# Kernel optimization log

Measured on AMD Instinct MI355X. Metric: run time of the kernel, lower is better.

Reference implementation:

```python
import jax, jax.numpy as jnp
import numpy as np

B, N, C = 4, 2048, 1024
H = 16
D = C // H  # head_dim = 64
SCALE = 1.0 / np.sqrt(D).astype(np.float32)


def setup_inputs() -> dict:
    key = jax.random.key(0)
    ks = jax.random.split(key, 6)
    s = 0.02
    return {
        "x": jax.random.normal(ks[0], (B, N, C), dtype=jnp.float32),
        "Wq": jax.random.normal(ks[1], (C, C), dtype=jnp.float32) * s,
        "Wk": jax.random.normal(ks[2], (C, C), dtype=jnp.float32) * s,
        "Wv": jax.random.normal(ks[3], (C, C), dtype=jnp.float32) * s,
        "Wo": jax.random.normal(ks[4], (C, C), dtype=jnp.float32) * s,
        "bo": jax.random.normal(ks[5], (C,), dtype=jnp.float32) * s,
    }


def reference(x, Wq, Wk, Wv, Wo, bo):
    # q/k/v projections (no bias, qkv_bias=False), split heads -> [B,H,N,D]
    def heads(t):
        return t.reshape(B, N, H, D).transpose(0, 2, 1, 3)
    q = heads(x @ Wq)
    k = heads(x @ Wk)
    v = heads(x @ Wv)
    attn = jnp.einsum("bhnd,bhmd->bhnm", q, k) * SCALE  # [B,H,N,N]
    attn = jax.nn.softmax(attn, axis=-1)
    out = jnp.einsum("bhnm,bhmd->bhnd", attn, v)  # [B,H,N,D]
    out = out.transpose(0, 2, 1, 3).reshape(B, N, C)
    return out @ Wo + bo
```

## Files before the change

### kernel.cpp

```cpp
#include <hip/hip_runtime.h>
#include <hip/hip_bf16.h>


typedef __bf16 bf16x8 __attribute__((ext_vector_type(8)));
typedef __bf16 bf16x4 __attribute__((ext_vector_type(4)));
typedef float  f32x4  __attribute__((ext_vector_type(4)));
typedef unsigned int u32x4 __attribute__((ext_vector_type(4)));

#define LSCALE 0.18033688f

__device__ __forceinline__ f32x4 mfma16(bf16x8 a, bf16x8 b, f32x4 c) {
    return __builtin_amdgcn_mfma_f32_16x16x32_bf16(a, b, c, 0, 0, 0);
}

__device__ __forceinline__ unsigned short f2bf(float f) {
    unsigned u = __builtin_bit_cast(unsigned, f);
    u += 0x7fffu + ((u >> 16) & 1u);
    return (unsigned short)(u >> 16);
}

__device__ __forceinline__ unsigned cvt_pk_bf16(float lo, float hi) {
    unsigned r;
    asm("v_cvt_pk_bf16_f32 %0, %1, %2" : "=v"(r) : "v"(lo), "v"(hi));
    return r;
}

__device__ __forceinline__ bf16x4 trread(unsigned addr) {
    bf16x4 d;
    asm volatile("ds_read_b64_tr_b16 %0, %1" : "=v"(d) : "v"(addr));
    return d;
}

__device__ __forceinline__ void gload16(const ushort* g, ushort* l) {
    __builtin_amdgcn_global_load_lds(
        (const __attribute__((address_space(1))) void*)g,
        (__attribute__((address_space(3))) void*)l, 16, 0, 0);
}

__global__ void cast_bf16_kernel(const float4* __restrict__ in,
                                 ushort4* __restrict__ out, int n4) {
    int i = blockIdx.x * blockDim.x + threadIdx.x;
    if (i < n4) {
        float4 f = in[i];
        ushort4 r;
        r.x = f2bf(f.x); r.y = f2bf(f.y); r.z = f2bf(f.z); r.w = f2bf(f.w);
        out[i] = r;
    }
}

__global__ void transpose_cast_kernel(const float* __restrict__ Wq,
                                      const float* __restrict__ Wk,
                                      const float* __restrict__ Wv,
                                      const float* __restrict__ Wo,
                                      ushort* __restrict__ out) {
    __shared__ float tile[32][33];
    const int z = blockIdx.z;
    const float* W = (z == 0) ? Wq : (z == 1) ? Wk : (z == 2) ? Wv : Wo;
    ushort* o = out + (size_t)z * 1024 * 1024;
    const int k0 = blockIdx.x * 32, n0 = blockIdx.y * 32;
    const int tx = threadIdx.x, ty = threadIdx.y;
#pragma unroll
    for (int i = 0; i < 4; i++)
        tile[ty + 8 * i][tx] = W[(size_t)(k0 + ty + 8 * i) * 1024 + n0 + tx];
    __syncthreads();
#pragma unroll
    for (int i = 0; i < 4; i++)
        o[(size_t)(n0 + ty + 8 * i) * 1024 + k0 + tx] = f2bf(tile[tx][ty + 8 * i]);
}

template <int MODE>
__global__ __launch_bounds__(256) void gemm128(const ushort* __restrict__ A,
                                               const ushort* __restrict__ Bt,
                                               ushort* __restrict__ outB,
                                               float* __restrict__ outF,
                                               const float* __restrict__ bias) {
    __shared__ ushort As[128 * 32];
    __shared__ ushort Bs[128 * 32];
    const int tid = threadIdx.x;
    const int lane = tid & 63;
    const int wid = tid >> 6;
    const int wm = wid >> 1, wn = wid & 1;
    const int m0 = blockIdx.x * 128;
    const int n0 = blockIdx.y * 128;
    if (MODE == 0) Bt += (size_t)blockIdx.z * (1024 * 1024);

    f32x4 acc[4][4] = {};

    for (int k0 = 0; k0 < 1024; k0 += 32) {
#pragma unroll
        for (int it = 0; it < 2; ++it) {
            int e = (it * 256 + tid) * 8;
            int r = e >> 5, c = e & 31;
            gload16(&A[(size_t)(m0 + r) * 1024 + k0 + c], &As[e]);
            gload16(&Bt[(size_t)(n0 + r) * 1024 + k0 + c], &Bs[e]);
        }
        __syncthreads();

        bf16x8 a[4], b[4];
#pragma unroll
        for (int i = 0; i < 4; i++) {
            a[i] = *(const bf16x8*)&As[(wm * 64 + i * 16 + (lane & 15)) * 32 + (lane >> 4) * 8];
            b[i] = *(const bf16x8*)&Bs[(wn * 64 + i * 16 + (lane & 15)) * 32 + (lane >> 4) * 8];
        }
#pragma unroll
        for (int i = 0; i < 4; i++)
#pragma unroll
            for (int j = 0; j < 4; j++)
                acc[i][j] = mfma16(a[i], b[j], acc[i][j]);
        __syncthreads();
    }

    const float scl = (MODE == 0 && blockIdx.z == 0) ? LSCALE : 1.0f;
#pragma unroll
    for (int i = 0; i < 4; i++) {
        int row_b = m0 + wm * 64 + i * 16 + ((lane >> 4) * 4);
#pragma unroll
        for (int j = 0; j < 4; j++) {
            int col = n0 + wn * 64 + j * 16 + (lane & 15);
#pragma unroll
            for (int r = 0; r < 4; r++) {
                int row = row_b + r;
                float v = acc[i][j][r] * scl;
                if (MODE == 0) {
                    ushort* o = outB + (size_t)blockIdx.z * (8192ull * 1024);
                    int b = row >> 11, n = row & 2047, h = col >> 6, d = col & 63;
                    o[((((size_t)(b * 16 + h)) * 2048 + n) << 6) + d] = f2bf(v);
                } else {
                    outF[(size_t)row * 1024 + col] = v + bias[col];
                }
            }
        }
    }
}

__global__ __launch_bounds__(256) void attn_kernel(const ushort* __restrict__ Q,
                                                   const ushort* __restrict__ K,
                                                   const ushort* __restrict__ V,
                                                   ushort* __restrict__ O) {
    __shared__ ushort Ks[64 * 64];
    __shared__ ushort Vs[64 * 64];
    __shared__ ushort Ps[4][2][1024];
    const int tid = threadIdx.x;
    const int lane = tid & 63;
    const int wid = tid >> 6;
    const int g = lane >> 4;
    const int q16 = lane & 15;
    const int bid = blockIdx.x;
    const int swz = (bid & 7) * 128 + (bid >> 3);
    const int bh = swz >> 4;
    const int qt = swz & 15;
    const size_t base = (size_t)bh * (2048 * 64);

    const int qr0 = qt * 128 + wid * 32 + q16;
    bf16x8 qf[2][2];
#pragma unroll
    for (int u = 0; u < 2; ++u)
#pragma unroll
        for (int ks = 0; ks < 2; ++ks)
            qf[u][ks] = *(const bf16x8*)&Q[base + (size_t)(qr0 + u * 16) * 64 + ks * 32 + g * 8];

    bf16x8 onesb;
#pragma unroll
    for (int i = 0; i < 8; i++) onesb[i] = (__bf16)1.0f;

    f32x4 o[2][4] = {};
    f32x4 lacc[2] = {};
    float m_run[2] = {-1e30f, -1e30f};

    char* KsB = (char*)Ks;
    const unsigned vb = (unsigned)(size_t)&Vs[0];

    for (int kt = 0; kt < 2048; kt += 64) {
#pragma unroll
        for (int it = 0; it < 2; ++it) {
            int ci = it * 256 + tid;
            int key = ci >> 3, d0 = (ci & 7) * 8;
            uint4 kv = *(const uint4*)&K[base + (size_t)(kt + key) * 64 + d0];
            int byt = (key * 128 + d0 * 2) ^ ((key & 7) << 4);
            *(uint4*)(KsB + byt) = kv;
        }
#pragma unroll
        for (int it = 0; it < 2; ++it) {
            int c = it * 256 + tid;
            int key = (c & 127) >> 1;
            int d0 = (c >> 7) * 16 + (c & 1) * 8;
            gload16(&V[base + (size_t)(kt + key) * 64 + d0], &Vs[c * 8]);
        }
        __syncthreads();

        f32x4 s[2][4] = {};
#pragma unroll
        for (int kb = 0; kb < 4; ++kb) {
#pragma unroll
            for (int ks = 0; ks < 2; ++ks) {
                int key = kb * 16 + q16;
                int d0 = ks * 32 + g * 8;
                int byt = (key * 128 + d0 * 2) ^ ((key & 7) << 4);
                bf16x8 kf = *(const bf16x8*)(KsB + byt);
                s[0][kb] = mfma16(kf, qf[0][ks], s[0][kb]);
                s[1][kb] = mfma16(kf, qf[1][ks], s[1][kb]);
            }
        }

        bf16x8 pa[2][2];
#pragma unroll
        for (int u = 0; u < 2; ++u) {
            float t[4][4];
#pragma unroll
            for (int kb = 0; kb < 4; ++kb)
#pragma unroll
                for (int r = 0; r < 4; ++r) t[kb][r] = s[u][kb][r];

            float mx = fmaxf(fmaxf(fmaxf(t[0][0], t[0][1]), fmaxf(t[0][2], t[0][3])),
                             fmaxf(fmaxf(t[1][0], t[1][1]), fmaxf(t[1][2], t[1][3])));
            mx = fmaxf(mx, fmaxf(fmaxf(fmaxf(t[2][0], t[2][1]), fmaxf(t[2][2], t[2][3])),
                                 fmaxf(fmaxf(t[3][0], t[3][1]), fmaxf(t[3][2], t[3][3]))));
            mx = fmaxf(mx, __shfl_xor(mx, 16));
            mx = fmaxf(mx, __shfl_xor(mx, 32));
            float mn = fmaxf(m_run[u], mx);
            float fr = __builtin_amdgcn_exp2f(m_run[u] - mn);
            m_run[u] = mn;

            unsigned w[4][2];
#pragma unroll
            for (int kb = 0; kb < 4; ++kb) {
                float p0 = __builtin_amdgcn_exp2f(t[kb][0] - mn);
                float p1 = __builtin_amdgcn_exp2f(t[kb][1] - mn);
                float p2 = __builtin_amdgcn_exp2f(t[kb][2] - mn);
                float p3 = __builtin_amdgcn_exp2f(t[kb][3] - mn);
                w[kb][0] = cvt_pk_bf16(p0, p1);
                w[kb][1] = cvt_pk_bf16(p2, p3);
            }

            char* PsB = (char*)Ps[wid][u];
            {
                u32x4 c0 = {w[0][0], w[0][1], w[2][0], w[2][1]};
                u32x4 c1 = {w[1][0], w[1][1], w[3][0], w[3][1]};
                *(u32x4*)(PsB + ((lane * 32 + 0)  ^ ((lane & 7) << 4))) = c0;
                *(u32x4*)(PsB + ((lane * 32 + 16) ^ ((lane & 7) << 4))) = c1;
            }
            asm volatile("" ::: "memory");
            __builtin_amdgcn_sched_barrier(0);
            int s1 = q16 + 32 * (g & 1);
            int ch = (g >> 1) * 16;
            u32x4 r1 = *(const u32x4*)(PsB + ((s1 * 32 + ch) ^ ((s1 & 7) << 4)));
            u32x4 r2 = *(const u32x4*)(PsB + (((s1 + 16) * 32 + ch) ^ (((s1 + 16) & 7) << 4)));
            asm volatile("" ::: "memory");
            {
                u32x4 p0 = {r1.x, r1.y, r2.x, r2.y};
                u32x4 p1 = {r1.z, r1.w, r2.z, r2.w};
                pa[u][0] = __builtin_bit_cast(bf16x8, p0);
                pa[u][1] = __builtin_bit_cast(bf16x8, p1);
            }

            float fro[4];
#pragma unroll
            for (int r = 0; r < 4; ++r) fro[r] = __shfl(fr, g * 4 + r);
#pragma unroll
            for (int cb = 0; cb < 4; ++cb)
#pragma unroll
                for (int r = 0; r < 4; ++r) o[u][cb][r] *= fro[r];
#pragma unroll
            for (int r = 0; r < 4; ++r) lacc[u][r] *= fro[r];

            lacc[u] = mfma16(pa[u][0], onesb, lacc[u]);
            lacc[u] = mfma16(pa[u][1], onesb, lacc[u]);
        }

        bf16x4 vlo[4][2], vhi[4][2];
#pragma unroll
        for (int cb = 0; cb < 4; ++cb)
#pragma unroll
            for (int ks = 0; ks < 2; ++ks) {
                unsigned a = vb + cb * 2048 + (ks * 32 + g * 8) * 32 + q16 * 8;
                vlo[cb][ks] = trread(a);
                vhi[cb][ks] = trread(a + 128);
            }
        asm volatile("s_waitcnt lgkmcnt(0)" ::: "memory");
        __builtin_amdgcn_sched_barrier(0);
#pragma unroll
        for (int cb = 0; cb < 4; ++cb)
#pragma unroll
            for (int ks = 0; ks < 2; ++ks) {
                bf16x8 vf = __builtin_shufflevector(vlo[cb][ks], vhi[cb][ks],
                                                    0, 1, 2, 3, 4, 5, 6, 7);
                o[0][cb] = mfma16(pa[0][ks], vf, o[0][cb]);
                o[1][cb] = mfma16(pa[1][ks], vf, o[1][cb]);
            }
        __syncthreads();
    }

    const int b = bh >> 4, h = bh & 15;
#pragma unroll
    for (int u = 0; u < 2; ++u) {
#pragma unroll
        for (int r = 0; r < 4; ++r) {
            float inv = 1.0f / lacc[u][r];
            int row = qt * 128 + wid * 32 + u * 16 + g * 4 + r;
#pragma unroll
            for (int cb = 0; cb < 4; ++cb) {
                int col = h * 64 + cb * 16 + q16;
                O[((size_t)(b * 2048 + row)) * 1024 + col] = f2bf(o[u][cb][r] * inv);
            }
        }
    }
}

extern "C" void kernel_launch(void* const* d_in, const int* in_sizes, int n_in,
                              void* d_out, int out_size, void* d_ws, size_t ws_size,
                              hipStream_t stream) {
    const float* x  = (const float*)d_in[0];
    const float* Wq = (const float*)d_in[1];
    const float* Wk = (const float*)d_in[2];
    const float* Wv = (const float*)d_in[3];
    const float* Wo = (const float*)d_in[4];
    const float* bo = (const float*)d_in[5];
    float* out = (float*)d_out;

    if (ws_size < (size_t)72 * 1024 * 1024) return;
    ushort* ws  = (ushort*)d_ws;
    ushort* xb  = ws;
    ushort* wt  = xb + (size_t)8 * 1024 * 1024;
    ushort* qkv = wt + (size_t)4 * 1024 * 1024;
    ushort* ao  = xb;

    cast_bf16_kernel<<<8192, 256, 0, stream>>>((const float4*)x, (ushort4*)xb,
                                               2 * 1024 * 1024);
    transpose_cast_kernel<<<dim3(32, 32, 4), dim3(32, 8), 0, stream>>>(Wq, Wk, Wv, Wo, wt);
    gemm128<0><<<dim3(64, 8, 3), 256, 0, stream>>>(xb, wt, qkv, nullptr, nullptr);
    attn_kernel<<<1024, 256, 0, stream>>>(
        qkv, qkv + (size_t)8 * 1024 * 1024, qkv + (size_t)16 * 1024 * 1024, ao);
    gemm128<1><<<dim3(64, 8, 1), 256, 0, stream>>>(ao, wt + (size_t)3 * 1024 * 1024,
                                                   nullptr, out, bo);
}
```

Measured before the change: 242.0 us.

## Double-buffer K/V tiles in attention kernel to overlap loads with compute

Doubles the shared-memory K and V buffers and prefetches the next key tile during the current tile's computation. V goes in through async global-to-LDS loads, while K is held in registers and written to LDS after the PV MFMAs. This drops one barrier per iteration and is meant to hide global-load latency behind the MFMA work. The cost is more LDS (which may lower occupancy) and more registers for the prefetched K values. A possible hazard is the shared-memory wait count when the async V loads mix with the LDS reads in the same iteration.

Result: faster. 237.0 us (-2.1%).

```diff
diff --git a/kernel.cpp b/kernel.cpp
--- a/kernel.cpp
+++ b/kernel.cpp
@@ -137,8 +137,8 @@
                                                    const ushort* __restrict__ K,
                                                    const ushort* __restrict__ V,
                                                    ushort* __restrict__ O) {
-    __shared__ ushort Ks[64 * 64];
-    __shared__ ushort Vs[64 * 64];
+    __shared__ ushort Ks[2][64 * 64];
+    __shared__ ushort Vs[2][64 * 64];
     __shared__ ushort Ps[4][2][1024];
     const int tid = threadIdx.x;
     const int lane = tid & 63;
@@ -167,26 +167,43 @@
     f32x4 lacc[2] = {};
     float m_run[2] = {-1e30f, -1e30f};
 
-    char* KsB = (char*)Ks;
-    const unsigned vb = (unsigned)(size_t)&Vs[0];
-
+    const int kci0 = tid, kci1 = 256 + tid;
+    const int kkey0 = kci0 >> 3, kd0 = (kci0 & 7) * 8;
+    const int kkey1 = kci1 >> 3, kd1 = (kci1 & 7) * 8;
+    const int kbyt0 = (kkey0 * 128 + kd0 * 2) ^ ((kkey0 & 7) << 4);
+    const int kbyt1 = (kkey1 * 128 + kd1 * 2) ^ ((kkey1 & 7) << 4);
+    const int vkey0 = (kci0 & 127) >> 1, vd0 = (kci0 >> 7) * 16 + (kci0 & 1) * 8;
+    const int vkey1 = (kci1 & 127) >> 1, vd1 = (kci1 >> 7) * 16 + (kci1 & 1) * 8;
+
+    char* const KsB0 = (char*)&Ks[0][0];
+    ushort* const Vs0 = &Vs[0][0];
+    const unsigned vb0 = (unsigned)(size_t)&Vs[0][0];
+
+    {
+        uint4 k0 = *(const uint4*)&K[base + (size_t)kkey0 * 64 + kd0];
+        uint4 k1 = *(const uint4*)&K[base + (size_t)kkey1 * 64 + kd1];
+        gload16(&V[base + (size_t)vkey0 * 64 + vd0], &Vs0[kci0 * 8]);
+        gload16(&V[base + (size_t)vkey1 * 64 + vd1], &Vs0[kci1 * 8]);
+        *(uint4*)(KsB0 + kbyt0) = k0;
+        *(uint4*)(KsB0 + kbyt1) = k1;
+    }
+    __syncthreads();
+
+    int cur = 0;
     for (int kt = 0; kt < 2048; kt += 64) {
-#pragma unroll
-        for (int it = 0; it < 2; ++it) {
-            int ci = it * 256 + tid;
-            int key = ci >> 3, d0 = (ci & 7) * 8;
-            uint4 kv = *(const uint4*)&K[base + (size_t)(kt + key) * 64 + d0];
-            int byt = (key * 128 + d0 * 2) ^ ((key & 7) << 4);
-            *(uint4*)(KsB + byt) = kv;
-        }
-#pragma unroll
-        for (int it = 0; it < 2; ++it) {
-            int c = it * 256 + tid;
-            int key = (c & 127) >> 1;
-            int d0 = (c >> 7) * 16 + (c & 1) * 8;
-            gload16(&V[base + (size_t)(kt + key) * 64 + d0], &Vs[c * 8]);
-        }
-        __syncthreads();
+        const int nxt = cur ^ 1;
+        const bool more = (kt + 64) < 2048;
+        char* const KsBc = KsB0 + cur * 8192;
+        const unsigned vbc = vb0 + cur * 8192;
+
+        uint4 kn0, kn1;
+        if (more) {
+            const size_t nb = base + (size_t)(kt + 64) * 64;
+            gload16(&V[nb + (size_t)vkey0 * 64 + vd0], &Vs0[nxt * 4096 + kci0 * 8]);
+            gload16(&V[nb + (size_t)vkey1 * 64 + vd1], &Vs0[nxt * 4096 + kci1 * 8]);
+            kn0 = *(const uint4*)&K[nb + (size_t)kkey0 * 64 + kd0];
+            kn1 = *(const uint4*)&K[nb + (size_t)kkey1 * 64 + kd1];
+        }
 
         f32x4 s[2][4] = {};
 #pragma unroll
@@ -196,7 +213,7 @@
                 int key = kb * 16 + q16;
                 int d0 = ks * 32 + g * 8;
                 int byt = (key * 128 + d0 * 2) ^ ((key & 7) << 4);
-                bf16x8 kf = *(const bf16x8*)(KsB + byt);
+                bf16x8 kf = *(const bf16x8*)(KsBc + byt);
                 s[0][kb] = mfma16(kf, qf[0][ks], s[0][kb]);
                 s[1][kb] = mfma16(kf, qf[1][ks], s[1][kb]);
             }
@@ -272,7 +289,7 @@
         for (int cb = 0; cb < 4; ++cb)
 #pragma unroll
             for (int ks = 0; ks < 2; ++ks) {
-                unsigned a = vb + cb * 2048 + (ks * 32 + g * 8) * 32 + q16 * 8;
+                unsigned a = vbc + cb * 2048 + (ks * 32 + g * 8) * 32 + q16 * 8;
                 vlo[cb][ks] = trread(a);
                 vhi[cb][ks] = trread(a + 128);
             }
@@ -287,7 +304,14 @@
                 o[0][cb] = mfma16(pa[0][ks], vf, o[0][cb]);
                 o[1][cb] = mfma16(pa[1][ks], vf, o[1][cb]);
             }
+
+        if (more) {
+            char* const KsBn = KsB0 + nxt * 8192;
+            *(uint4*)(KsBn + kbyt0) = kn0;
+            *(uint4*)(KsBn + kbyt1) = kn1;
+        }
         __syncthreads();
+        cur = nxt;
     }
 
     const int b = bh >> 4, h = bh & 15;
```
